# Kernel tuning notes

Hardware: AMD Instinct MI355X
Metric: run time of the kernel (lower is better)

The kernel has to match this reference:

```python
import jax, jax.numpy as jnp
import numpy as np

L = 24        # n_layer
E = 1024      # n_emb
H = 4 * E     # ffn hidden
V = 50277     # vocab
LN_EPS = 1e-5


def _ln(x, w, b):
    m = x.mean(-1, keepdims=True)
    v = ((x - m) ** 2).mean(-1, keepdims=True)
    return (x - m) / jnp.sqrt(v + LN_EPS) * w + b


def setup_inputs() -> dict:
    key = jax.random.key(0)
    ks = jax.random.split(key, 24)
    s = 1.0 / np.sqrt(E)      # keep matvec outputs O(1) so exp-recurrence is stable
    sh = 1.0 / np.sqrt(H)
    inp = {
        "emb":      jax.random.normal(ks[0], (V, E), jnp.float32) * 0.02,
        "ln0_w":    jnp.ones((E,), jnp.float32),
        "ln0_b":    jnp.zeros((E,), jnp.float32),
        "ln1_w":    jnp.ones((L, E), jnp.float32),
        "ln1_b":    jnp.zeros((L, E), jnp.float32),
        "att_tmk":  jax.random.uniform(ks[1], (L, E), jnp.float32),
        "att_tmv":  jax.random.uniform(ks[2], (L, E), jnp.float32),
        "att_tmr":  jax.random.uniform(ks[3], (L, E), jnp.float32),
        "att_tf":   jax.random.normal(ks[4], (L, E), jnp.float32) * 0.3,
        # checkpoint stores raw time_decay; loader applies -exp(.)
        "att_td":   -jnp.exp(jax.random.normal(ks[5], (L, E), jnp.float32) * 0.3),
        "att_kw":   jax.random.normal(ks[6], (L, E, E), jnp.float32) * s,
        "att_vw":   jax.random.normal(ks[7], (L, E, E), jnp.float32) * s,
        "att_rw":   jax.random.normal(ks[8], (L, E, E), jnp.float32) * s,
        "att_ow":   jax.random.normal(ks[9], (L, E, E), jnp.float32) * s,
        "ln2_w":    jnp.ones((L, E), jnp.float32),
        "ln2_b":    jnp.zeros((L, E), jnp.float32),
        "ffn_tmk":  jax.random.uniform(ks[10], (L, E), jnp.float32),
        "ffn_tmr":  jax.random.uniform(ks[11], (L, E), jnp.float32),
        "ffn_kw":   jax.random.normal(ks[12], (L, H, E), jnp.float32) * s,
        "ffn_vw":   jax.random.normal(ks[13], (L, E, H), jnp.float32) * sh,
        "ffn_rw":   jax.random.normal(ks[14], (L, E, E), jnp.float32) * s,
        "ln_out_w": jnp.ones((E,), jnp.float32),
        "ln_out_b": jnp.zeros((E,), jnp.float32),
        "head_w":   jax.random.normal(ks[15], (V, E), jnp.float32) * s,
        "token":    123,
    }
    state = jnp.zeros((5 * L, E), jnp.float32)
    state = state.at[4::5].set(-1e30)  # pp slot, as in empty_state()
    inp["state"] = state
    return inp


def _rwkv_forward(emb, ln0_w, ln0_b, ln1_w, ln1_b, att_tmk, att_tmv, att_tmr,
                  att_tf, att_td, att_kw, att_vw, att_rw, att_ow,
                  ln2_w, ln2_b, ffn_tmk, ffn_tmr, ffn_kw, ffn_vw, ffn_rw,
                  ln_out_w, ln_out_b, head_w, state, token):
    x = emb[token]
    x = _ln(x, ln0_w, ln0_b)           # blocks.0.ln0 applied once before layer 0
    st = state.reshape(L, 5, E)        # slots: (ffn_x, att_x, aa, bb, pp)

    def step(x, inp):
        (s, l1w, l1b, tmk, tmv, tmr, tf, td, kw, vw, rw, ow,
         l2w, l2b, ftmk, ftmr, fkw, fvw, frw) = inp
        ffn_x, att_x, aa, bb, pp = s[0], s[1], s[2], s[3], s[4]
        # --- time-mix (SA) ---
        xn = _ln(x, l1w, l1b)
        xk = xn * tmk + att_x * (1 - tmk)
        xv = xn * tmv + att_x * (1 - tmv)
        xr = xn * tmr + att_x * (1 - tmr)
        r = jax.nn.sigmoid(rw @ xr)
        k = kw @ xk
        v = vw @ xv
        # numerically-stabilized WKV output
        ww = tf + k
        p = jnp.maximum(pp, ww)
        e1 = jnp.exp(pp - p)
        e2 = jnp.exp(ww - p)
        a = e1 * aa + e2 * v
        b = e1 * bb + e2
        # state update
        ww2 = pp + td
        p2 = jnp.maximum(ww2, k)
        f1 = jnp.exp(ww2 - p2)
        f2 = jnp.exp(k - p2)
        naa = f1 * aa + f2 * v
        nbb = f1 * bb + f2
        npp = p2
        sx = x + ow @ (r * a / b)
        # --- channel-mix (FF) ---
        xn2 = _ln(sx, l2w, l2b)
        fxk = xn2 * ftmk + ffn_x * (1 - ftmk)
        fxr = xn2 * ftmr + ffn_x * (1 - ftmr)
        fr = jax.nn.sigmoid(frw @ fxr)
        fk = jnp.square(jax.nn.relu(fkw @ fxk))
        out = sx + fr * (fvw @ fk)
        new_s = jnp.stack([xn2, xn, naa, nbb, npp])
        return out, new_s

    xs = (st, ln1_w, ln1_b, att_tmk, att_tmv, att_tmr, att_tf, att_td,
          att_kw, att_vw, att_rw, att_ow, ln2_w, ln2_b, ffn_tmk, ffn_tmr,
          ffn_kw, ffn_vw, ffn_rw)
    x, new_st = jax.lax.scan(step, x, xs)
    logits = head_w @ _ln(x, ln_out_w, ln_out_b)
    return logits, new_st.reshape(5 * L, E)


def reference(emb, ln0_w, ln0_b, ln1_w, ln1_b, att_tmk, att_tmv, att_tmr,
              att_tf, att_td, att_kw, att_vw, att_rw, att_ow,
              ln2_w, ln2_b, ffn_tmk, ffn_tmr, ffn_kw, ffn_vw, ffn_rw,
              ln_out_w, ln_out_b, head_w, state, token):
    return _rwkv_forward(emb, ln0_w, ln0_b, ln1_w, ln1_b, att_tmk, att_tmv,
                         att_tmr, att_tf, att_td, att_kw, att_vw, att_rw,
                         att_ow, ln2_w, ln2_b, ffn_tmk, ffn_tmr, ffn_kw,
                         ffn_vw, ffn_rw, ln_out_w, ln_out_b, head_w,
                         state, token)
```

## Files before the change

### kernel.cpp

```cpp
#include <hip/hip_runtime.h>

#define E 1024
#define H 4096
#define NLAYER 24
#define V 50277
#define NB 256
#define NT 1024
#define LN_EPS 1e-5f

typedef unsigned long long u64;

#define R1O    0
#define R2O    16384
#define POOLO  32768
#define SXO    36864
#define SSXO   37888
#define FXRO   38912
#define REDO   39936
#define PARTO  39968
#define PART2O 39984
#define SMEMF  40000

struct Params {
  const float* emb;   const float* ln0_w; const float* ln0_b;
  const float* ln1_w; const float* ln1_b;
  const float* tmk;   const float* tmv;   const float* tmr;
  const float* tf;    const float* td;
  const float* kw;    const float* vw;    const float* rw;  const float* ow;
  const float* ln2_w; const float* ln2_b;
  const float* ftmk;  const float* ftmr;
  const float* fkw;   const float* fvw;   const float* frw;
  const float* lnow;  const float* lnob;  const float* headw;
  const float* st;    const int* tok;
  float* out; float* ws;
};

__device__ __forceinline__ void stg_tag(u64* p, float v, unsigned tag) {
  u64 w = ((u64)__float_as_uint(v) << 32) | (u64)tag;
  __hip_atomic_store(p, w, __ATOMIC_RELAXED, __HIP_MEMORY_SCOPE_AGENT);
}
__device__ __forceinline__ u64 ld_tag(const u64* p) {
  return __hip_atomic_load(p, __ATOMIC_RELAXED, __HIP_MEMORY_SCOPE_AGENT);
}
__device__ __forceinline__ float poll_tag(const u64* p, unsigned tag) {
  u64 w = ld_tag(p);
  while ((unsigned)w != tag) { __builtin_amdgcn_s_sleep(1); w = ld_tag(p); }
  return __uint_as_float((unsigned)(w >> 32));
}

__device__ __forceinline__ void wait_pf() {
  asm volatile("s_waitcnt vmcnt(0)" ::: "memory");
}

__device__ __forceinline__ void gload_lds16(const float* g, float* l) {
  __builtin_amdgcn_global_load_lds(
      (const __attribute__((address_space(1))) unsigned int*)(g),
      (__attribute__((address_space(3))) unsigned int*)(l), 16, 0, 0);
}
__device__ __forceinline__ void pf_row4k(const float* row, float* dst, int lane) {
#pragma unroll
  for (int c = 0; c < 4; ++c)
    gload_lds16(row + c * 256 + lane * 4, dst + c * 256);
}

__device__ __forceinline__ float warp_sum(float v) {
#pragma unroll
  for (int off = 32; off; off >>= 1) v += __shfl_down(v, off);
  return v;
}

__device__ __forceinline__ float2 ln_stats(float v, float* red) {
  float a = v, b = v * v;
#pragma unroll
  for (int off = 32; off; off >>= 1) { a += __shfl_xor(a, off); b += __shfl_xor(b, off); }
  const int wid = threadIdx.x >> 6, lane = threadIdx.x & 63;
  if (lane == 0) { red[2 * wid] = a; red[2 * wid + 1] = b; }
  __syncthreads();
  float s1 = 0.f, s2 = 0.f;
  const float2* r2 = (const float2*)red;
#pragma unroll
  for (int j = 0; j < 16; ++j) { float2 t = r2[j]; s1 += t.x; s2 += t.y; }
  float m = s1 * (1.f / E);
  return make_float2(m, s2 * (1.f / E) - m * m);
}

__device__ __forceinline__ float dot4(float4 a, float4 b) {
  return a.x * b.x + a.y * b.y + a.z * b.z + a.w * b.w;
}

__device__ __forceinline__ float dotlds(const float* wrow, const float* vec, int lane) {
  const float4* w4 = (const float4*)wrow;
  const float4* v4 = (const float4*)vec;
  float acc = 0.f;
#pragma unroll
  for (int p = 0; p < 4; ++p)
    acc += dot4(w4[lane + p * 64], v4[lane + p * 64]);
  return warp_sum(acc);
}

__global__ __launch_bounds__(NT, 1) void rwkv_kernel(Params p) {
  const int tid = threadIdx.x, bid = blockIdx.x;
  const int lane = tid & 63, wid = tid >> 6;

  extern __shared__ float smem[];
  float* r1     = smem + R1O;
  float* r2     = smem + R2O;
  float* pool   = smem + POOLO;
  float* s_x    = smem + SXO;
  float* s_sx   = smem + SSXO;
  float* s_fxr  = smem + FXRO;
  float* s_red  = smem + REDO;
  float* s_part = smem + PARTO;
  float* s_part2= smem + PART2O;

  u64* tws = (u64*)p.ws;
  u64* tk  = tws;
  u64* tv  = tws + 2 * E;
  u64* tr  = tws + 4 * E;
  u64* tsx = tws + 6 * E;
  u64* tx  = tws + 8 * E;
  u64* tfk = tws + 10 * E;

  float* out_st = p.out + V;
  const int token = p.tok[0];

  const bool hasA = wid < 12;
  const int rA = bid * 12 + wid;
  const int matA = rA >> 10, rmA = rA & (E - 1);
  const int rloc = wid >> 2, kc = wid & 3;
  const int rowO = bid * 4 + rloc;
  float* wA = r1 + wid * 1024;
  float* wD = r2 + rloc * 4096 + kc * 1024;

  if (hasA) {
    const float* W = (matA == 0 ? p.kw : matA == 1 ? p.vw : p.rw) + (size_t)rmA * E;
    pf_row4k(W, wA, lane);
  }

  {
    float v = p.emb[(size_t)token * E + tid];
    float2 mv = ln_stats(v, s_red);
    s_x[tid] = (v - mv.x) / sqrtf(mv.y + LN_EPS) * p.ln0_w[tid] + p.ln0_b[tid];
  }

  for (int l = 0; l < NLAYER; ++l) {
    const float* stl = p.st + (size_t)5 * l * E;
    float* ostl = out_st + (size_t)5 * l * E;
    const int par = l & 1;
    const unsigned tg = (unsigned)(l + 1);

    float l1w = p.ln1_w[l * E + tid], l1b = p.ln1_b[l * E + tid];
    float ax = stl[E + tid];
    float ta = p.tmk[l * E + tid], tb = p.tmv[l * E + tid], tc = p.tmr[l * E + tid];
    float xv_;
    if (l > 0) { xv_ = poll_tag(&tx[par * E + tid], (unsigned)l); s_x[tid] = xv_; }
    else       { xv_ = s_x[tid]; }
    {
      float2 mv = ln_stats(xv_, s_red);
      float xn = (xv_ - mv.x) / sqrtf(mv.y + LN_EPS) * l1w + l1b;
      pool[tid]        = xn * ta + ax * (1.f - ta);
      pool[1024 + tid] = xn * tb + ax * (1.f - tb);
      pool[2048 + tid] = xn * tc + ax * (1.f - tc);
      if (bid == 0) ostl[E + tid] = xn;
    }
    __syncthreads();
    wait_pf();
    if (hasA) {
      float d = dotlds(wA, pool + matA * 1024, lane);
      if (lane == 0) {
        u64* dst = (matA == 0 ? tk : matA == 1 ? tv : tr) + par * E + rmA;
        stg_tag(dst, matA == 2 ? 1.f / (1.f + expf(-d)) : d, tg);
      }
    }

    {
      float aav = stl[2 * E + tid], bbv = stl[3 * E + tid], ppv = stl[4 * E + tid];
      float tfv = p.tf[l * E + tid], tdv = p.td[l * E + tid];
      float4 wow = ((const float4*)(p.ow + (size_t)l * E * E + (size_t)rowO * E + kc * 256))[lane];
      pf_row4k(p.fkw + (size_t)l * H * E + (size_t)(bid * 16 + wid) * E, wA, lane);
      const u64 *bk = tk + par * E + tid, *bv = tv + par * E + tid, *br = tr + par * E + tid;
      u64 wk = ld_tag(bk), wv = ld_tag(bv), wr = ld_tag(br);
      while ((unsigned)wk != tg) { __builtin_amdgcn_s_sleep(1); wk = ld_tag(bk); }
      while ((unsigned)wv != tg) { __builtin_amdgcn_s_sleep(1); wv = ld_tag(bv); }
      while ((unsigned)wr != tg) { __builtin_amdgcn_s_sleep(1); wr = ld_tag(br); }
      float kk = __uint_as_float((unsigned)(wk >> 32));
      float vv = __uint_as_float((unsigned)(wv >> 32));
      float rr = __uint_as_float((unsigned)(wr >> 32));
      float wwv = tfv + kk;
      float pm = fmaxf(ppv, wwv);
      float e1 = expf(ppv - pm), e2 = expf(wwv - pm);
      float a = e1 * aav + e2 * vv, b = e1 * bbv + e2;
      pool[3072 + tid] = rr * a / b;
      float ww2 = ppv + tdv;
      float p2 = fmaxf(ww2, kk);
      float f1 = expf(ww2 - p2), f2 = expf(kk - p2);
      if (bid == 0) {
        ostl[2 * E + tid] = f1 * aav + f2 * vv;
        ostl[3 * E + tid] = f1 * bbv + f2;
        ostl[4 * E + tid] = p2;
      }
      __syncthreads();
      const float4* v4 = (const float4*)(pool + 3072 + kc * 256);
      float acc = warp_sum(dot4(wow, v4[lane]));
      if (lane == 0) s_part[wid] = acc;
    }
    __syncthreads();
    if (tid < 4) {
      float dsum = s_part[tid * 4] + s_part[tid * 4 + 1] +
                   s_part[tid * 4 + 2] + s_part[tid * 4 + 3];
      stg_tag(&tsx[par * E + bid * 4 + tid], s_x[bid * 4 + tid] + dsum, tg);
    }

    {
      float l2w = p.ln2_w[l * E + tid], l2b = p.ln2_b[l * E + tid];
      float fx = stl[tid];
      float fa = p.ftmk[l * E + tid], fb = p.ftmr[l * E + tid];
      float4 wfr = ((const float4*)(p.frw + (size_t)l * E * E + (size_t)rowO * E + kc * 256))[lane];
      pf_row4k(p.fvw + (size_t)l * E * H + (size_t)rowO * H + kc * 1024, wD, lane);
      float sxv = poll_tag(&tsx[par * E + tid], tg);
      s_sx[tid] = sxv;
      float2 mv = ln_stats(sxv, s_red);
      float xn2 = (sxv - mv.x) / sqrtf(mv.y + LN_EPS) * l2w + l2b;
      pool[tid]  = xn2 * fa + fx * (1.f - fa);
      s_fxr[tid] = xn2 * fb + fx * (1.f - fb);
      if (bid == 0) ostl[tid] = xn2;
      __syncthreads();
      float d = dotlds(wA, pool, lane);
      if (lane == 0) { float t = fmaxf(d, 0.f); stg_tag(&tfk[par * H + bid * 16 + wid], t * t, tg); }
      const float4* f4 = (const float4*)(s_fxr + kc * 256);
      float fp = warp_sum(dot4(wfr, f4[lane]));
      if (lane == 0) s_part2[wid] = fp;
    }

    if (l + 1 < NLAYER && hasA) {
      const float* W = (matA == 0 ? p.kw : matA == 1 ? p.vw : p.rw) +
                       (size_t)(l + 1) * E * E + (size_t)rmA * E;
      pf_row4k(W, wA, lane);
    }
    __syncthreads();
    {
      const u64* base = tfk + par * H;
      u64 w0 = ld_tag(base + tid);
      u64 w1 = ld_tag(base + tid + 1024);
      u64 w2 = ld_tag(base + tid + 2048);
      u64 w3 = ld_tag(base + tid + 3072);
      while ((unsigned)w0 != tg) { __builtin_amdgcn_s_sleep(1); w0 = ld_tag(base + tid); }
      while ((unsigned)w1 != tg) { __builtin_amdgcn_s_sleep(1); w1 = ld_tag(base + tid + 1024); }
      while ((unsigned)w2 != tg) { __builtin_amdgcn_s_sleep(1); w2 = ld_tag(base + tid + 2048); }
      while ((unsigned)w3 != tg) { __builtin_amdgcn_s_sleep(1); w3 = ld_tag(base + tid + 3072); }
      pool[tid]        = __uint_as_float((unsigned)(w0 >> 32));
      pool[tid + 1024] = __uint_as_float((unsigned)(w1 >> 32));
      pool[tid + 2048] = __uint_as_float((unsigned)(w2 >> 32));
      pool[tid + 3072] = __uint_as_float((unsigned)(w3 >> 32));
    }
    __syncthreads();
    {
      const float4* v4 = (const float4*)(pool + kc * 1024);
      const float4* w4 = (const float4*)wD;
      float acc = 0.f;
#pragma unroll
      for (int pc = 0; pc < 4; ++pc)
        acc += dot4(w4[lane + pc * 64], v4[lane + pc * 64]);
      acc = warp_sum(acc);
      if (lane == 0) s_part[wid] = acc;
    }
    __syncthreads();
    if (tid < 4) {
      float dsum = s_part[tid * 4] + s_part[tid * 4 + 1] +
                   s_part[tid * 4 + 2] + s_part[tid * 4 + 3];
      float frs  = s_part2[tid * 4] + s_part2[tid * 4 + 1] +
                   s_part2[tid * 4 + 2] + s_part2[tid * 4 + 3];
      float fr = 1.f / (1.f + expf(-frs));
      stg_tag(&tx[((l + 1) & 1) * E + bid * 4 + tid],
              s_sx[bid * 4 + tid] + fr * dsum, tg);
    }
  }

  {
    float xv_ = poll_tag(&tx[(NLAYER & 1) * E + tid], (unsigned)NLAYER);
    float2 mv = ln_stats(xv_, s_red);
    pool[tid] = (xv_ - mv.x) / sqrtf(mv.y + LN_EPS) * p.lnow[tid] + p.lnob[tid];
  }
  __syncthreads();
  {
    const int gw = bid * 16 + wid;
    const float4* v4 = (const float4*)pool;
    int row = gw;
    for (; row + 4096 < V; row += 8192) {
      const float4* W0 = (const float4*)(p.headw + (size_t)row * E);
      const float4* W1 = (const float4*)(p.headw + (size_t)(row + 4096) * E);
      float a0 = 0.f, a1 = 0.f;
#pragma unroll
      for (int pc = 0; pc < 4; ++pc) {
        float4 x = v4[lane + pc * 64];
        a0 += dot4(W0[lane + pc * 64], x);
        a1 += dot4(W1[lane + pc * 64], x);
      }
      a0 = warp_sum(a0); a1 = warp_sum(a1);
      if (lane == 0) { p.out[row] = a0; p.out[row + 4096] = a1; }
    }
    for (; row < V; row += 4096) {
      const float4* W0 = (const float4*)(p.headw + (size_t)row * E);
      float a0 = 0.f;
#pragma unroll
      for (int pc = 0; pc < 4; ++pc)
        a0 += dot4(W0[lane + pc * 64], v4[lane + pc * 64]);
      a0 = warp_sum(a0);
      if (lane == 0) p.out[row] = a0;
    }
  }
}

extern "C" void kernel_launch(void* const* d_in, const int* in_sizes, int n_in,
                              void* d_out, int out_size, void* d_ws, size_t ws_size,
                              hipStream_t stream) {
  Params p;
  p.emb   = (const float*)d_in[0];
  p.ln0_w = (const float*)d_in[1];
  p.ln0_b = (const float*)d_in[2];
  p.ln1_w = (const float*)d_in[3];
  p.ln1_b = (const float*)d_in[4];
  p.tmk   = (const float*)d_in[5];
  p.tmv   = (const float*)d_in[6];
  p.tmr   = (const float*)d_in[7];
  p.tf    = (const float*)d_in[8];
  p.td    = (const float*)d_in[9];
  p.kw    = (const float*)d_in[10];
  p.vw    = (const float*)d_in[11];
  p.rw    = (const float*)d_in[12];
  p.ow    = (const float*)d_in[13];
  p.ln2_w = (const float*)d_in[14];
  p.ln2_b = (const float*)d_in[15];
  p.ftmk  = (const float*)d_in[16];
  p.ftmr  = (const float*)d_in[17];
  p.fkw   = (const float*)d_in[18];
  p.fvw   = (const float*)d_in[19];
  p.frw   = (const float*)d_in[20];
  p.lnow  = (const float*)d_in[21];
  p.lnob  = (const float*)d_in[22];
  p.headw = (const float*)d_in[23];
  if (in_sizes[24] == 1) {
    p.tok = (const int*)d_in[24];
    p.st  = (const float*)d_in[25];
  } else {
    p.st  = (const float*)d_in[24];
    p.tok = (const int*)d_in[25];
  }
  p.out   = (float*)d_out;
  p.ws    = (float*)d_ws;

  hipMemsetAsync(d_ws, 0, (10 * E + 2 * H) * sizeof(unsigned long long), stream);

  void* args[] = { &p };
  hipLaunchCooperativeKernel((const void*)rwkv_kernel, dim3(NB), dim3(NT),
                             args, SMEMF * sizeof(float), stream);
}
```

Baseline: 554.3 us.

## Prefetch output-projection rows to LDS and drop cross-warp reduction barriers

Attention output-projection rows are now prefetched into spare LDS slots (warps 12-15 of r1) during the previous layer, instead of loaded from global memory on the critical path. The output projection and the FFN value matvec are each done by four warps computing whole rows, which removes the shared-memory partial-sum step and one __syncthreads per stage. The state writeback is spread across all blocks rather than done by block 0 alone. In exchange, the critical matvecs run on fewer warps with longer serial dot products, and the fkw prefetch for warps 12-15 is deferred until after the output projection.

Result: slower. 580.7 us (+4.8%).

```diff
diff --git a/kernel.cpp b/kernel.cpp
--- a/kernel.cpp
+++ b/kernel.cpp
@@ -110,7 +110,6 @@
   float* s_sx   = smem + SSXO;
   float* s_fxr  = smem + FXRO;
   float* s_red  = smem + REDO;
-  float* s_part = smem + PARTO;
   float* s_part2= smem + PART2O;
 
   u64* tws = (u64*)p.ws;
@@ -129,6 +128,8 @@
   const int matA = rA >> 10, rmA = rA & (E - 1);
   const int rloc = wid >> 2, kc = wid & 3;
   const int rowO = bid * 4 + rloc;
+  const int rowW = bid * 4 + wid;
+  const bool ownE = (tid >> 2) == bid;
   float* wA = r1 + wid * 1024;
   float* wD = r2 + rloc * 4096 + kc * 1024;
 
@@ -136,6 +137,8 @@
     const float* W = (matA == 0 ? p.kw : matA == 1 ? p.vw : p.rw) + (size_t)rmA * E;
     pf_row4k(W, wA, lane);
   }
+  if (wid < 4)
+    pf_row4k(p.ow + (size_t)rowW * E, r1 + (12 + wid) * 1024, lane);
 
   {
     float v = p.emb[(size_t)token * E + tid];
@@ -161,7 +164,7 @@
       pool[tid]        = xn * ta + ax * (1.f - ta);
       pool[1024 + tid] = xn * tb + ax * (1.f - tb);
       pool[2048 + tid] = xn * tc + ax * (1.f - tc);
-      if (bid == 0) ostl[E + tid] = xn;
+      if (ownE) ostl[E + tid] = xn;
     }
     __syncthreads();
     wait_pf();
@@ -176,8 +179,8 @@
     {
       float aav = stl[2 * E + tid], bbv = stl[3 * E + tid], ppv = stl[4 * E + tid];
       float tfv = p.tf[l * E + tid], tdv = p.td[l * E + tid];
-      float4 wow = ((const float4*)(p.ow + (size_t)l * E * E + (size_t)rowO * E + kc * 256))[lane];
-      pf_row4k(p.fkw + (size_t)l * H * E + (size_t)(bid * 16 + wid) * E, wA, lane);
+      if (wid < 12)
+        pf_row4k(p.fkw + (size_t)l * H * E + (size_t)(bid * 16 + wid) * E, wA, lane);
       const u64 *bk = tk + par * E + tid, *bv = tv + par * E + tid, *br = tr + par * E + tid;
       u64 wk = ld_tag(bk), wv = ld_tag(bv), wr = ld_tag(br);
       while ((unsigned)wk != tg) { __builtin_amdgcn_s_sleep(1); wk = ld_tag(bk); }
@@ -194,22 +197,26 @@
       float ww2 = ppv + tdv;
       float p2 = fmaxf(ww2, kk);
       float f1 = expf(ww2 - p2), f2 = expf(kk - p2);
-      if (bid == 0) {
+      if (ownE) {
         ostl[2 * E + tid] = f1 * aav + f2 * vv;
         ostl[3 * E + tid] = f1 * bbv + f2;
         ostl[4 * E + tid] = p2;
       }
       __syncthreads();
-      const float4* v4 = (const float4*)(pool + 3072 + kc * 256);
-      float acc = warp_sum(dot4(wow, v4[lane]));
-      if (lane == 0) s_part[wid] = acc;
+      if (wid < 4) {
+        const float4* w4 = (const float4*)(r1 + (12 + wid) * 1024);
+        const float4* v4 = (const float4*)(pool + 3072);
+        float acc = 0.f;
+#pragma unroll
+        for (int pc = 0; pc < 4; ++pc)
+          acc += dot4(w4[lane + pc * 64], v4[lane + pc * 64]);
+        acc = warp_sum(acc);
+        if (lane == 0) stg_tag(&tsx[par * E + rowW], s_x[rowW] + acc, tg);
+      }
     }
     __syncthreads();
-    if (tid < 4) {
-      float dsum = s_part[tid * 4] + s_part[tid * 4 + 1] +
-                   s_part[tid * 4 + 2] + s_part[tid * 4 + 3];
-      stg_tag(&tsx[par * E + bid * 4 + tid], s_x[bid * 4 + tid] + dsum, tg);
-    }
+    if (wid >= 12)
+      pf_row4k(p.fkw + (size_t)l * H * E + (size_t)(bid * 16 + wid) * E, wA, lane);
 
     {
       float l2w = p.ln2_w[l * E + tid], l2b = p.ln2_b[l * E + tid];
@@ -223,7 +230,7 @@
       float xn2 = (sxv - mv.x) / sqrtf(mv.y + LN_EPS) * l2w + l2b;
       pool[tid]  = xn2 * fa + fx * (1.f - fa);
       s_fxr[tid] = xn2 * fb + fx * (1.f - fb);
-      if (bid == 0) ostl[tid] = xn2;
+      if (ownE) ostl[tid] = xn2;
       __syncthreads();
       float d = dotlds(wA, pool, lane);
       if (lane == 0) { float t = fmaxf(d, 0.f); stg_tag(&tfk[par * H + bid * 16 + wid], t * t, tg); }
@@ -254,26 +261,24 @@
       pool[tid + 3072] = __uint_as_float((unsigned)(w3 >> 32));
     }
     __syncthreads();
-    {
-      const float4* v4 = (const float4*)(pool + kc * 1024);
-      const float4* w4 = (const float4*)wD;
+    if (wid < 4) {
+      const float4* w4 = (const float4*)(r2 + wid * 4096);
+      const float4* v4 = (const float4*)pool;
       float acc = 0.f;
 #pragma unroll
-      for (int pc = 0; pc < 4; ++pc)
+      for (int pc = 0; pc < 16; ++pc)
         acc += dot4(w4[lane + pc * 64], v4[lane + pc * 64]);
       acc = warp_sum(acc);
-      if (lane == 0) s_part[wid] = acc;
-    }
-    __syncthreads();
-    if (tid < 4) {
-      float dsum = s_part[tid * 4] + s_part[tid * 4 + 1] +
-                   s_part[tid * 4 + 2] + s_part[tid * 4 + 3];
-      float frs  = s_part2[tid * 4] + s_part2[tid * 4 + 1] +
-                   s_part2[tid * 4 + 2] + s_part2[tid * 4 + 3];
-      float fr = 1.f / (1.f + expf(-frs));
-      stg_tag(&tx[((l + 1) & 1) * E + bid * 4 + tid],
-              s_sx[bid * 4 + tid] + fr * dsum, tg);
-    }
+      if (lane == 0) {
+        float frs = s_part2[wid * 4] + s_part2[wid * 4 + 1] +
+                    s_part2[wid * 4 + 2] + s_part2[wid * 4 + 3];
+        float fr = 1.f / (1.f + expf(-frs));
+        stg_tag(&tx[((l + 1) & 1) * E + rowW], s_sx[rowW] + fr * acc, tg);
+      }
+    }
+    if (l + 1 < NLAYER && wid < 4)
+      pf_row4k(p.ow + (size_t)(l + 1) * E * E + (size_t)rowW * E,
+               r1 + (12 + wid) * 1024, lane);
   }
 
   {
```
